# Optimization experiments

Hardware: AMD Instinct MI355X
Metric: run time of the kernel (lower is better)

The kernel has to match this reference:

```python
import jax, jax.numpy as jnp
import numpy as np

M = 0.5
S = 64.0
LS_EPS = 0.0
COS_M = float(np.cos(M))
SIN_M = float(np.sin(M))
THRESHOLD = float(np.cos(np.pi - M))
MM = float(np.sin(np.pi - M) * M)
N_CLASSES = 100000


def setup_inputs() -> dict:
    key = jax.random.key(0)
    k1, k2, k3 = jax.random.split(key, 3)
    embeddings = jax.random.normal(k1, (1024, 512), dtype=jnp.float32)
    kernel = jax.random.normal(k2, (512, N_CLASSES), dtype=jnp.float32) * 0.01
    t = jnp.zeros((1,), dtype=jnp.float32)
    label = jax.random.randint(k3, (1024,), 0, N_CLASSES, dtype=jnp.int64)
    return {"embeddings": embeddings, "kernel": kernel, "t": t, "label": label}


def reference(embeddings, kernel, t, label):
    # l2-normalize embeddings over feature axis, kernel over input axis
    emb = embeddings / jnp.linalg.norm(embeddings, axis=1, keepdims=True)
    kn = kernel / jnp.linalg.norm(kernel, axis=0, keepdims=True)
    cos_theta = jnp.clip(emb @ kn, -1.0, 1.0)  # [N, C]
    n = embeddings.shape[0]
    rows = jnp.arange(n)
    target_logit = cos_theta[rows, label][:, None]  # [N, 1]
    sin_theta = jnp.sqrt(1.0 - target_logit ** 2)
    cos_theta_m = target_logit * COS_M - sin_theta * SIN_M  # [N, 1]
    mask = cos_theta > cos_theta_m  # hard examples (broadcast per row)
    final_target_logit = jnp.where(target_logit > THRESHOLD,
                                   cos_theta_m, target_logit - MM)
    # running-mean buffer update (no-grad in original)
    t_new = jax.lax.stop_gradient(target_logit.mean() * 0.01 + 0.99 * t[0])
    cos_theta = jnp.where(mask, cos_theta * (t_new + cos_theta), cos_theta)
    cos_theta = cos_theta.at[rows, label].set(final_target_logit[:, 0])
    if LS_EPS > 0:
        cos_theta = (1 - LS_EPS) * cos_theta + LS_EPS / N_CLASSES
    return cos_theta * S
```

## Files before the change

### kernel.cpp

```cpp
#include <hip/hip_runtime.h>

typedef unsigned short u16;
typedef unsigned int u32;
typedef __attribute__((ext_vector_type(8))) short bf16x8;
typedef __attribute__((ext_vector_type(4))) float f32x4;

#define KDIM   512
#define NROWS  1024
#define NCLS   100000
#define CPAD   100096
#define NSTRIP 391
#define NMT    4
#define NWG    (NSTRIP*NMT)

#define COS_M_C   0.8775825618903728f
#define SIN_M_C   0.4794255386042030f
#define THRESH_C  (-0.8775825618903728f)
#define MM_C      0.2397127693021015f
#define S_C       64.0f

__device__ __forceinline__ u16 f2bf(float f) {
    u32 x = __float_as_uint(f);
    x += 0x7fffu + ((x >> 16) & 1u);
    return (u16)(x >> 16);
}
__device__ __forceinline__ float bf2f(u16 u) {
    return __uint_as_float(((u32)u) << 16);
}
__device__ __forceinline__ u32 pack2(float a, float b) {
    return (u32)f2bf(a) | ((u32)f2bf(b) << 16);
}

__device__ __forceinline__ void gld16(const void* g, void* l) {
    __builtin_amdgcn_global_load_lds(
        (const __attribute__((address_space(1))) void*)g,
        (__attribute__((address_space(3))) void*)l, 16, 0, 0);
}


__global__ __launch_bounds__(64)
void norm_emb_k(const float* __restrict__ emb, float* __restrict__ Af,
                u16* __restrict__ Aw) {
    const int i = blockIdx.x, l = threadIdx.x;
    const float* e = emb + i * KDIM;
    float4 v0 = *(const float4*)(e + l * 8);
    float4 v1 = *(const float4*)(e + l * 8 + 4);
    float s = v0.x*v0.x + v0.y*v0.y + v0.z*v0.z + v0.w*v0.w
            + v1.x*v1.x + v1.y*v1.y + v1.z*v1.z + v1.w*v1.w;
    #pragma unroll
    for (int o = 1; o < 64; o <<= 1) s += __shfl_xor(s, o);
    float inv = rsqrtf(s);
    float4 n0 = make_float4(v0.x*inv, v0.y*inv, v0.z*inv, v0.w*inv);
    float4 n1 = make_float4(v1.x*inv, v1.y*inv, v1.z*inv, v1.w*inv);
    *(float4*)(Af + i*KDIM + l*8)     = n0;
    *(float4*)(Af + i*KDIM + l*8 + 4) = n1;
    const int mt = i >> 8, row = i & 255;
    uint4 w;
    w.x = pack2(n0.x, n0.y);
    w.y = pack2(n0.z, n0.w);
    w.z = pack2(n1.x, n1.y);
    w.w = pack2(n1.z, n1.w);
    *(uint4*)(Aw + mt*131072 + (l>>3)*16384 + row*64
              + (((l&7) + row) & 7) * 8) = w;
}

__global__ __launch_bounds__(256)
void transpose_norm_k(const float* __restrict__ Kg, u16* __restrict__ Bn,
                      float* __restrict__ kinv) {
    __shared__ float Ls[32 * 260];
    const int t  = threadIdx.x;
    const int jb = blockIdx.x * 256;
    const int j  = jb + t;
    u16* bstrip = Bn + (size_t)blockIdx.x * 131072;
    float acc = 0.f;
    for (int kc = 0; kc < 16; ++kc) {
        #pragma unroll
        for (int it = 0; it < 8; ++it) {
            int fid  = it * 256 + t;
            int r    = fid >> 6;
            int c4   = (fid & 63) * 4;
            int gcol = jb + c4;
            float4 v;
            if (gcol + 3 < NCLS) {
                v = *(const float4*)(Kg + (kc*32 + r) * NCLS + gcol);
            } else {
                v.x = (gcol + 0 < NCLS) ? Kg[(kc*32 + r)*NCLS + gcol + 0] : 0.f;
                v.y = (gcol + 1 < NCLS) ? Kg[(kc*32 + r)*NCLS + gcol + 1] : 0.f;
                v.z = (gcol + 2 < NCLS) ? Kg[(kc*32 + r)*NCLS + gcol + 2] : 0.f;
                v.w = (gcol + 3 < NCLS) ? Kg[(kc*32 + r)*NCLS + gcol + 3] : 0.f;
            }
            *(float4*)(Ls + r * 260 + c4) = v;
        }
        __syncthreads();
        #pragma unroll
        for (int sub = 0; sub < 4; ++sub) {
            u16 u[8];
            #pragma unroll
            for (int e = 0; e < 8; ++e) {
                float v = Ls[(sub*8 + e) * 260 + t];
                acc += v * v;
                u[e] = f2bf(v);
            }
            uint4 w;
            w.x = (u32)u[0] | ((u32)u[1] << 16);
            w.y = (u32)u[2] | ((u32)u[3] << 16);
            w.z = (u32)u[4] | ((u32)u[5] << 16);
            w.w = (u32)u[6] | ((u32)u[7] << 16);
            *(uint4*)(bstrip + (kc>>1)*16384 + t*64
                      + ((((kc&1)*4 + sub) + t) & 7) * 8) = w;
        }
        __syncthreads();
    }
    kinv[j] = rsqrtf(fmaxf(acc, 1e-30f));
}

__global__ __launch_bounds__(64)
void target_k(const float* __restrict__ Af, const u16* __restrict__ Bn,
              const float* __restrict__ kinv, const int* __restrict__ label,
              float* __restrict__ tgt, float* __restrict__ ctm,
              float* __restrict__ fin) {
    const int i = blockIdx.x, l = threadIdx.x;
    const int lab = label[i];
    const int kbase = (l >> 3) * 64 + (l & 7) * 8;
    float4 a0 = *(const float4*)(Af + i * KDIM + kbase);
    float4 a1 = *(const float4*)(Af + i * KDIM + kbase + 4);
    const int col = lab & 255;
    uint4 bv = *(const uint4*)(Bn + (size_t)(lab >> 8) * 131072
               + (l >> 3) * 16384 + col * 64 + (((l & 7) + col) & 7) * 8);
    float d = a0.x * bf2f((u16)(bv.x & 0xffff)) + a0.y * bf2f((u16)(bv.x >> 16))
            + a0.z * bf2f((u16)(bv.y & 0xffff)) + a0.w * bf2f((u16)(bv.y >> 16))
            + a1.x * bf2f((u16)(bv.z & 0xffff)) + a1.y * bf2f((u16)(bv.z >> 16))
            + a1.z * bf2f((u16)(bv.w & 0xffff)) + a1.w * bf2f((u16)(bv.w >> 16));
    #pragma unroll
    for (int o = 1; o < 64; o <<= 1) d += __shfl_xor(d, o);
    if (l == 0) {
        float c = d * kinv[lab];
        c = fminf(fmaxf(c, -1.f), 1.f);
        tgt[i] = c;
        float sn = sqrtf(fmaxf(1.f - c*c, 0.f));
        float cm = c * COS_M_C - sn * SIN_M_C;
        ctm[i] = cm;
        fin[i] = (c > THRESH_C) ? cm : (c - MM_C);
    }
}

__global__ __launch_bounds__(256)
void tnew_k(const float* __restrict__ tgt, const float* __restrict__ tin,
            float* __restrict__ tnw) {
    __shared__ float red[256];
    const int t = threadIdx.x;
    float s = tgt[t] + tgt[t + 256] + tgt[t + 512] + tgt[t + 768];
    red[t] = s;
    __syncthreads();
    for (int o = 128; o > 0; o >>= 1) {
        if (t < o) red[t] += red[t + o];
        __syncthreads();
    }
    if (t == 0) tnw[0] = red[0] * (0.01f / 1024.f) + 0.99f * tin[0];
}

__global__ __launch_bounds__(512, 2)
void gemm_k(const u16* __restrict__ A, const u16* __restrict__ B,
            const float* __restrict__ kinv, const float* __restrict__ ctm,
            const float* __restrict__ fin, const int* __restrict__ label,
            const float* __restrict__ tnwp, float* __restrict__ out) {
    __shared__ __align__(16) u16 As[2][16384];
    __shared__ __align__(16) u16 Bs[2][16384];
    const int tid  = threadIdx.x;
    const int wave = tid >> 6, lane = tid & 63;

    const int L   = blockIdx.x;
    const int xcd = L & 7;
    const int wg  = (xcd < 4 ? xcd * 196 : 784 + (xcd - 4) * 195) + (L >> 3);
    const int mt  = wg & 3;
    const int cs  = wg >> 2;
    const int m0  = mt * 256;
    const int j0  = cs * 256;
    const int wrl = (wave >> 2) * 128;
    const int wcl = (wave & 3) * 64;

    f32x4 acc[8][4] = {};

    const u16* gA = A + mt * 131072 + tid * 8;
    const u16* gB = B + (size_t)cs * 131072 + tid * 8;
    const int  ld = tid * 8;

    const int rowA = wrl + (lane & 15);
    const int colB = wcl + (lane & 15);
    const int qh   = lane >> 4;
    const int aOff0 = rowA * 64 + ((qh     + rowA) & 7) * 8;
    const int aOff1 = rowA * 64 + ((qh + 4 + rowA) & 7) * 8;
    const int bOff0 = colB * 64 + ((qh     + colB) & 7) * 8;
    const int bOff1 = colB * 64 + ((qh + 4 + colB) & 7) * 8;

#define STAGE(b, kt) do {                                        \
    gld16(gA + (kt)*16384 +     0, &As[b][ld]);                  \
    gld16(gA + (kt)*16384 +  4096, &As[b][ld + 4096]);           \
    gld16(gA + (kt)*16384 +  8192, &As[b][ld + 8192]);           \
    gld16(gA + (kt)*16384 + 12288, &As[b][ld + 12288]);          \
    gld16(gB + (kt)*16384 +     0, &Bs[b][ld]);                  \
    gld16(gB + (kt)*16384 +  4096, &Bs[b][ld + 4096]);           \
    gld16(gB + (kt)*16384 +  8192, &Bs[b][ld + 8192]);           \
    gld16(gB + (kt)*16384 + 12288, &Bs[b][ld + 12288]);          \
} while (0)

    STAGE(0, 0);
    #pragma unroll 2
    for (int kt = 0; kt < 8; ++kt) {
        const int cur = kt & 1;
        if (kt < 7) {
            STAGE(cur ^ 1, kt + 1);
            asm volatile("s_waitcnt vmcnt(8)" ::: "memory");
        } else {
            asm volatile("s_waitcnt vmcnt(0)" ::: "memory");
        }
        __builtin_amdgcn_s_barrier();
        __builtin_amdgcn_sched_barrier(0);

        const u16* a = As[cur];
        const u16* b = Bs[cur];
        bf16x8 af[8], bfr[4];

        #pragma unroll
        for (int m = 0; m < 8; ++m)
            af[m] = *(const bf16x8*)(a + aOff0 + m * 1024);
        #pragma unroll
        for (int n = 0; n < 4; ++n)
            bfr[n] = *(const bf16x8*)(b + bOff0 + n * 1024);
        asm volatile("s_waitcnt lgkmcnt(0)" ::: "memory");
        __builtin_amdgcn_sched_barrier(0);
        __builtin_amdgcn_s_setprio(1);
        #pragma unroll
        for (int m = 0; m < 8; ++m)
            #pragma unroll
            for (int n = 0; n < 4; ++n)
                acc[m][n] = __builtin_amdgcn_mfma_f32_16x16x32_bf16(
                                af[m], bfr[n], acc[m][n], 0, 0, 0);
        __builtin_amdgcn_s_setprio(0);

        #pragma unroll
        for (int m = 0; m < 8; ++m)
            af[m] = *(const bf16x8*)(a + aOff1 + m * 1024);
        #pragma unroll
        for (int n = 0; n < 4; ++n)
            bfr[n] = *(const bf16x8*)(b + bOff1 + n * 1024);
        asm volatile("s_waitcnt lgkmcnt(0)" ::: "memory");
        __builtin_amdgcn_sched_barrier(0);
        __builtin_amdgcn_s_barrier();
        __builtin_amdgcn_sched_barrier(0);
        __builtin_amdgcn_s_setprio(1);
        #pragma unroll
        for (int m = 0; m < 8; ++m)
            #pragma unroll
            for (int n = 0; n < 4; ++n)
                acc[m][n] = __builtin_amdgcn_mfma_f32_16x16x32_bf16(
                                af[m], bfr[n], acc[m][n], 0, 0, 0);
        __builtin_amdgcn_s_setprio(0);
    }
#undef STAGE

    const float tnew = *tnwp;
    const int colbase = j0 + wcl + (lane & 15);
    float kv[4];
    int cols[4];
    #pragma unroll
    for (int n = 0; n < 4; ++n) {
        cols[n] = colbase + n * 16;
        kv[n] = kinv[cols[n]];
    }
    #pragma unroll
    for (int m = 0; m < 8; ++m) {
        const int rb = m0 + wrl + m * 16 + (lane >> 4) * 4;
        #pragma unroll
        for (int r = 0; r < 4; ++r) {
            const int row = rb + r;
            const int lab = label[row];
            const float ct = ctm[row];
            const float fv = fin[row];
            float* orow = out + (size_t)row * NCLS;
            #pragma unroll
            for (int n = 0; n < 4; ++n) {
                float c = acc[m][n][r] * kv[n];
                c = fminf(fmaxf(c, -1.f), 1.f);
                float v = (c > ct) ? c * (tnew + c) : c;
                v = (cols[n] == lab) ? fv : v;
                if (cols[n] < NCLS)
                    orow[cols[n]] = v * S_C;
            }
        }
    }
}

extern "C" void kernel_launch(void* const* d_in, const int* in_sizes, int n_in,
                              void* d_out, int out_size, void* d_ws, size_t ws_size,
                              hipStream_t stream) {
    const float* emb = (const float*)d_in[0];
    const float* Kg  = (const float*)d_in[1];
    const float* tin = (const float*)d_in[2];
    const int*   lab = (const int*)d_in[3];
    float* out = (float*)d_out;

    char* w = (char*)d_ws;
    u16*   Bn   = (u16*)w;
    u16*   Aw   = (u16*)(w + 102498304);
    float* Af   = (float*)(w + 103546880);
    float* kinv = (float*)(w + 105644032);
    float* tgt  = (float*)(w + 106044416);
    float* ctmv = (float*)(w + 106048512);
    float* finv = (float*)(w + 106052608);
    float* tnw  = (float*)(w + 106056704);

    norm_emb_k<<<NROWS, 64, 0, stream>>>(emb, Af, Aw);
    transpose_norm_k<<<NSTRIP, 256, 0, stream>>>(Kg, Bn, kinv);
    target_k<<<NROWS, 64, 0, stream>>>(Af, Bn, kinv, lab, tgt, ctmv, finv);
    tnew_k<<<1, 256, 0, stream>>>(tgt, tin, tnw);
    gemm_k<<<NWG, 512, 0, stream>>>(
        Aw, Bn, kinv, ctmv, finv, lab, tnw, out);
}
```

Before: 388.3 us.

## Use 4-stage K32 LDS pipeline with new packed B/A image layout

Changes the preformatted bf16 A and B image layout to 32-wide K chunks with a new swizzle (imgoff), and restructures the GEMM main loop from a 2-buffer K64 double buffer into a 4-slot ring with 3 stages in flight, with waits counted per stage. LDS per block stays at 128KB but launch bounds now target one block per CU. Fragment loads are split so the second half of A loads overlaps the first MFMA group. The aim is to hide global load latency better. The cost is fewer resident blocks and more barriers per tile.

```diff
diff --git a/kernel.cpp b/kernel.cpp
--- a/kernel.cpp
+++ b/kernel.cpp
@@ -29,6 +29,10 @@
 }
 __device__ __forceinline__ u32 pack2(float a, float b) {
     return (u32)f2bf(a) | ((u32)f2bf(b) << 16);
+}
+
+__device__ __forceinline__ int imgoff(int r, int q) {
+    return (r >> 1) * 64 + ((((r & 1) << 2) + q + (r >> 1)) & 7) * 8;
 }
 
 __device__ __forceinline__ void gld16(const void* g, void* l) {
@@ -60,8 +64,7 @@
     w.y = pack2(n0.z, n0.w);
     w.z = pack2(n1.x, n1.y);
     w.w = pack2(n1.z, n1.w);
-    *(uint4*)(Aw + mt*131072 + (l>>3)*16384 + row*64
-              + (((l&7) + row) & 7) * 8) = w;
+    *(uint4*)(Aw + mt*131072 + (l>>2)*8192 + imgoff(row, l & 3)) = w;
 }
 
 __global__ __launch_bounds__(256)
@@ -93,11 +96,11 @@
         }
         __syncthreads();
         #pragma unroll
-        for (int sub = 0; sub < 4; ++sub) {
+        for (int q = 0; q < 4; ++q) {
             u16 u[8];
             #pragma unroll
             for (int e = 0; e < 8; ++e) {
-                float v = Ls[(sub*8 + e) * 260 + t];
+                float v = Ls[(q*8 + e) * 260 + t];
                 acc += v * v;
                 u[e] = f2bf(v);
             }
@@ -106,8 +109,7 @@
             w.y = (u32)u[2] | ((u32)u[3] << 16);
             w.z = (u32)u[4] | ((u32)u[5] << 16);
             w.w = (u32)u[6] | ((u32)u[7] << 16);
-            *(uint4*)(bstrip + (kc>>1)*16384 + t*64
-                      + ((((kc&1)*4 + sub) + t) & 7) * 8) = w;
+            *(uint4*)(bstrip + kc*8192 + imgoff(t, q)) = w;
         }
         __syncthreads();
     }
@@ -121,12 +123,10 @@
               float* __restrict__ fin) {
     const int i = blockIdx.x, l = threadIdx.x;
     const int lab = label[i];
-    const int kbase = (l >> 3) * 64 + (l & 7) * 8;
-    float4 a0 = *(const float4*)(Af + i * KDIM + kbase);
-    float4 a1 = *(const float4*)(Af + i * KDIM + kbase + 4);
-    const int col = lab & 255;
+    float4 a0 = *(const float4*)(Af + i * KDIM + l * 8);
+    float4 a1 = *(const float4*)(Af + i * KDIM + l * 8 + 4);
     uint4 bv = *(const uint4*)(Bn + (size_t)(lab >> 8) * 131072
-               + (l >> 3) * 16384 + col * 64 + (((l & 7) + col) & 7) * 8);
+               + (l >> 2) * 8192 + imgoff(lab & 255, l & 3));
     float d = a0.x * bf2f((u16)(bv.x & 0xffff)) + a0.y * bf2f((u16)(bv.x >> 16))
             + a0.z * bf2f((u16)(bv.y & 0xffff)) + a0.w * bf2f((u16)(bv.y >> 16))
             + a1.x * bf2f((u16)(bv.z & 0xffff)) + a1.y * bf2f((u16)(bv.z >> 16))
@@ -159,13 +159,12 @@
     if (t == 0) tnw[0] = red[0] * (0.01f / 1024.f) + 0.99f * tin[0];
 }
 
-__global__ __launch_bounds__(512, 2)
+__global__ __launch_bounds__(512, 1)
 void gemm_k(const u16* __restrict__ A, const u16* __restrict__ B,
             const float* __restrict__ kinv, const float* __restrict__ ctm,
             const float* __restrict__ fin, const int* __restrict__ label,
             const float* __restrict__ tnwp, float* __restrict__ out) {
-    __shared__ __align__(16) u16 As[2][16384];
-    __shared__ __align__(16) u16 Bs[2][16384];
+    __shared__ __align__(16) u16 S[4][16384];
     const int tid  = threadIdx.x;
     const int wave = tid >> 6, lane = tid & 63;
 
@@ -176,85 +175,71 @@
     const int cs  = wg >> 2;
     const int m0  = mt * 256;
     const int j0  = cs * 256;
-    const int wrl = (wave >> 2) * 128;
-    const int wcl = (wave & 3) * 64;
+    const int wm  = wave >> 2;
+    const int wn  = wave & 3;
+    const int wrl = wm * 128;
+    const int wcl = wn * 64;
 
     f32x4 acc[8][4] = {};
 
     const u16* gA = A + mt * 131072 + tid * 8;
     const u16* gB = B + (size_t)cs * 131072 + tid * 8;
-    const int  ld = tid * 8;
-
-    const int rowA = wrl + (lane & 15);
-    const int colB = wcl + (lane & 15);
-    const int qh   = lane >> 4;
-    const int aOff0 = rowA * 64 + ((qh     + rowA) & 7) * 8;
-    const int aOff1 = rowA * 64 + ((qh + 4 + rowA) & 7) * 8;
-    const int bOff0 = colB * 64 + ((qh     + colB) & 7) * 8;
-    const int bOff1 = colB * 64 + ((qh + 4 + colB) & 7) * 8;
-
-#define STAGE(b, kt) do {                                        \
-    gld16(gA + (kt)*16384 +     0, &As[b][ld]);                  \
-    gld16(gA + (kt)*16384 +  4096, &As[b][ld + 4096]);           \
-    gld16(gA + (kt)*16384 +  8192, &As[b][ld + 8192]);           \
-    gld16(gA + (kt)*16384 + 12288, &As[b][ld + 12288]);          \
-    gld16(gB + (kt)*16384 +     0, &Bs[b][ld]);                  \
-    gld16(gB + (kt)*16384 +  4096, &Bs[b][ld + 4096]);           \
-    gld16(gB + (kt)*16384 +  8192, &Bs[b][ld + 8192]);           \
-    gld16(gB + (kt)*16384 + 12288, &Bs[b][ld + 12288]);          \
+
+    const int lr = lane & 15, q = lane >> 4;
+    const int aB = imgoff(wrl + lr, q);
+    const int bB = 8192 + imgoff(wcl + lr, q);
+
+#define STAGE(s) do {                                            \
+    gld16(gA + (s)*8192,        &S[(s)&3][tid*8]);               \
+    gld16(gA + (s)*8192 + 4096, &S[(s)&3][tid*8 + 4096]);        \
+    gld16(gB + (s)*8192,        &S[(s)&3][8192  + tid*8]);       \
+    gld16(gB + (s)*8192 + 4096, &S[(s)&3][12288 + tid*8]);       \
 } while (0)
 
-    STAGE(0, 0);
-    #pragma unroll 2
-    for (int kt = 0; kt < 8; ++kt) {
-        const int cur = kt & 1;
-        if (kt < 7) {
-            STAGE(cur ^ 1, kt + 1);
-            asm volatile("s_waitcnt vmcnt(8)" ::: "memory");
-        } else {
-            asm volatile("s_waitcnt vmcnt(0)" ::: "memory");
-        }
+    STAGE(0); STAGE(1); STAGE(2);
+    #pragma unroll
+    for (int s = 0; s < 16; ++s) {
+        __builtin_amdgcn_s_barrier();
+        if (s + 3 < 16) STAGE(s + 3);
+        if (s <= 12)      asm volatile("s_waitcnt vmcnt(12)" ::: "memory");
+        else if (s == 13) asm volatile("s_waitcnt vmcnt(8)"  ::: "memory");
+        else if (s == 14) asm volatile("s_waitcnt vmcnt(4)"  ::: "memory");
+        else              asm volatile("s_waitcnt vmcnt(0)"  ::: "memory");
         __builtin_amdgcn_s_barrier();
         __builtin_amdgcn_sched_barrier(0);
 
-        const u16* a = As[cur];
-        const u16* b = Bs[cur];
-        bf16x8 af[8], bfr[4];
-
-        #pragma unroll
-        for (int m = 0; m < 8; ++m)
-            af[m] = *(const bf16x8*)(a + aOff0 + m * 1024);
+        const u16* sa = S[s & 3];
+        bf16x8 af[4], bf[4], af2[4];
+        #pragma unroll
+        for (int m = 0; m < 4; ++m)
+            af[m]  = *(const bf16x8*)(sa + aB + m * 512);
         #pragma unroll
         for (int n = 0; n < 4; ++n)
-            bfr[n] = *(const bf16x8*)(b + bOff0 + n * 1024);
+            bf[n]  = *(const bf16x8*)(sa + bB + n * 512);
+        #pragma unroll
+        for (int m = 0; m < 4; ++m)
+            af2[m] = *(const bf16x8*)(sa + aB + 2048 + m * 512);
+
+        asm volatile("s_waitcnt lgkmcnt(4)" ::: "memory");
+        __builtin_amdgcn_sched_barrier(0);
+        __builtin_amdgcn_s_setprio(1);
+        #pragma unroll
+        for (int m = 0; m < 4; ++m)
+            #pragma unroll
+            for (int n = 0; n < 4; ++n)
+                acc[m][n] = __builtin_amdgcn_mfma_f32_16x16x32_bf16(
+                                af[m], bf[n], acc[m][n], 0, 0, 0);
+        __builtin_amdgcn_s_setprio(0);
+
         asm volatile("s_waitcnt lgkmcnt(0)" ::: "memory");
         __builtin_amdgcn_sched_barrier(0);
         __builtin_amdgcn_s_setprio(1);
         #pragma unroll
-        for (int m = 0; m < 8; ++m)
+        for (int m = 0; m < 4; ++m)
             #pragma unroll
             for (int n = 0; n < 4; ++n)
-                acc[m][n] = __builtin_amdgcn_mfma_f32_16x16x32_bf16(
-                                af[m], bfr[n], acc[m][n], 0, 0, 0);
-        __builtin_amdgcn_s_setprio(0);
-
-        #pragma unroll
-        for (int m = 0; m < 8; ++m)
-            af[m] = *(const bf16x8*)(a + aOff1 + m * 1024);
-        #pragma unroll
-        for (int n = 0; n < 4; ++n)
-            bfr[n] = *(const bf16x8*)(b + bOff1 + n * 1024);
-        asm volatile("s_waitcnt lgkmcnt(0)" ::: "memory");
-        __builtin_amdgcn_sched_barrier(0);
-        __builtin_amdgcn_s_barrier();
-        __builtin_amdgcn_sched_barrier(0);
-        __builtin_amdgcn_s_setprio(1);
-        #pragma unroll
-        for (int m = 0; m < 8; ++m)
-            #pragma unroll
-            for (int n = 0; n < 4; ++n)
-                acc[m][n] = __builtin_amdgcn_mfma_f32_16x16x32_bf16(
-                                af[m], bfr[n], acc[m][n], 0, 0, 0);
+                acc[4 + m][n] = __builtin_amdgcn_mfma_f32_16x16x32_bf16(
+                                af2[m], bf[n], acc[4 + m][n], 0, 0, 0);
         __builtin_amdgcn_s_setprio(0);
     }
 #undef STAGE
```

Result: faster. 354.7 us (-8.7%).
